# Optimization experiments

Measured on AMD Instinct MI355X. Metric: run time of the kernel, lower is better.

## Reference

```python
import jax, jax.numpy as jnp
import numpy as np

E, W, S, Q, D = 256, 20, 5, 300, 512
ALPHA = 37.0  # hardcoded weight '37' in computeProto


def setup_inputs() -> dict:
    key = jax.random.key(0)
    k1, k2 = jax.random.split(key)
    x_shot = jax.random.normal(k1, (E, W, S, D), dtype=jnp.float32)
    x_query = jax.random.normal(k2, (E, Q, D), dtype=jnp.float32)
    temp = jnp.float32(10.0)
    return {"x_shot": x_shot, "x_query": x_query, "temp": temp}


def compute_proto(x_shot, x_query):
    # x_shot: [E, W, S, D], x_query: [E, Q, D]
    n_shot = x_shot.shape[2]
    shot_sum = x_shot.sum(axis=2)                      # [E, W, D]
    shot_mean = x_shot.mean(axis=2)                    # [E, W, D]
    # pairwise euclidean distance mean-vs-query: [E, W, Q]
    diff = shot_mean[:, :, None, :] - x_query[:, None, :, :]
    dist = jnp.sqrt(jnp.sum(diff * diff, axis=-1))
    weights = jax.nn.softmax(-dist, axis=-1)           # softmax over queries
    pooled = jnp.einsum('ewq,eqd->ewd', weights, x_query)  # [E, W, D]
    proto = (shot_sum + ALPHA * pooled) / (n_shot + ALPHA)
    return proto


def l2norm(x, axis=-1, eps=1e-12):
    n = jnp.sqrt(jnp.sum(x * x, axis=axis, keepdims=True))
    return x / jnp.maximum(n, eps)


def reference(x_shot, x_query, temp):
    proto = compute_proto(x_shot, x_query)             # [E, W, D]
    proto = l2norm(proto)
    q = l2norm(x_query)
    logits = temp * jnp.einsum('eqd,ewd->eqw', q, proto)  # [E, Q, W]
    return logits
```

## Files before the change

kernel.cpp:

```cpp
#include <hip/hip_runtime.h>
#include <math.h>

#define E_ 256
#define W_ 20
#define S_ 5
#define Q_ 300
#define D_ 512
#define ALPHA_ 37.0f
#define QCH 64
#define NCH 5
#define QPAD 304

typedef __attribute__((ext_vector_type(8))) short bf16x8;
typedef __attribute__((ext_vector_type(4))) float f32x4;
typedef __attribute__((ext_vector_type(2))) unsigned int u32x2;
typedef __attribute__((ext_vector_type(4))) unsigned int u32x4;

#define OFF_SS   0
#define OFF_XQ   32768
#define OFF_BUF  98304
#define OFF_Q2   122624
#define OFF_M2   123904
#define OFF_RED  124032
#define LDS_BYTES 124672

__device__ __forceinline__ unsigned short f2bf(float x) {
    unsigned int u = __builtin_bit_cast(unsigned int, x);
    u += 0x7fffu + ((u >> 16) & 1u);
    return (unsigned short)(u >> 16);
}
__device__ __forceinline__ float bf2f(unsigned short h) {
    unsigned int u = ((unsigned int)h) << 16;
    return __builtin_bit_cast(float, u);
}

__device__ __forceinline__ bf16x8 ldfrag(const char* base, int row, int k0) {
    const int phys = (k0 >> 3) ^ (row & 7);
    return *reinterpret_cast<const bf16x8*>(base + row * 1024 + phys * 16);
}

__device__ __forceinline__ void stage_load(const float4* xq4, int c, int qcount,
                                           int tid, float4* r) {
    const int qr = tid >> 3;
    const int i  = tid & 7;
    const int qg = c * QCH + ((qr < qcount) ? qr : 0);
    const float4* row4 = xq4 + (size_t)qg * (D_ / 4);
    #pragma unroll
    for (int j = 0; j < 8; ++j) {
        const int ch = i + 8 * j;
        r[2 * j]     = row4[2 * ch];
        r[2 * j + 1] = row4[2 * ch + 1];
    }
}

template <bool WQ2>
__device__ __forceinline__ void stage_write(const float4* r, char* s_xq, float* s_q2,
                                            int c, int qcount, int tid) {
    const int qr = tid >> 3;
    const int i  = tid & 7;
    const bool valid = qr < qcount;
    float q2 = 0.f;
    #pragma unroll
    for (int j = 0; j < 8; ++j) {
        const int ch = i + 8 * j;
        float4 a = valid ? r[2 * j]     : make_float4(0.f, 0.f, 0.f, 0.f);
        float4 b = valid ? r[2 * j + 1] : make_float4(0.f, 0.f, 0.f, 0.f);
        if (WQ2) {
            q2 += a.x * a.x + a.y * a.y + a.z * a.z + a.w * a.w
                + b.x * b.x + b.y * b.y + b.z * b.z + b.w * b.w;
        }
        u32x4 v;
        v[0] = (unsigned int)f2bf(a.x) | ((unsigned int)f2bf(a.y) << 16);
        v[1] = (unsigned int)f2bf(a.z) | ((unsigned int)f2bf(a.w) << 16);
        v[2] = (unsigned int)f2bf(b.x) | ((unsigned int)f2bf(b.y) << 16);
        v[3] = (unsigned int)f2bf(b.z) | ((unsigned int)f2bf(b.w) << 16);
        *reinterpret_cast<u32x4*>(s_xq + qr * 1024 + ((ch ^ (qr & 7)) << 4)) = v;
    }
    if (WQ2) {
        q2 += __shfl_xor(q2, 1);
        q2 += __shfl_xor(q2, 2);
        q2 += __shfl_xor(q2, 4);
        if (i == 0) s_q2[c * QCH + qr] = valid ? q2 : 0.f;
    }
}

__global__ __launch_bounds__(512) void fused5(const float* __restrict__ xs,
                                              const float* __restrict__ xq,
                                              const float* __restrict__ temp_p,
                                              float* __restrict__ out) {
    extern __shared__ char smem[];
    char*  s_ss  = smem + OFF_SS;
    char*  s_xq  = smem + OFF_XQ;
    float* s_buf = (float*)(smem + OFF_BUF);
    float* s_q2  = (float*)(smem + OFF_Q2);
    float* s_m2  = (float*)(smem + OFF_M2);
    float* s_red = (float*)(smem + OFF_RED);

    const int e    = blockIdx.x;
    const int tid  = threadIdx.x;
    const int lane = tid & 63;
    const int wv   = tid >> 6;
    const int ln15 = lane & 15;
    const int hi   = lane >> 4;

    const float*  xse = xs + (size_t)e * (W_ * S_ * D_);
    const float*  xqe = xq + (size_t)e * (Q_ * D_);
    const float4* xq4 = (const float4*)xqe;
    const float   temp = *temp_p;

    float4 buf[16];

    stage_load(xq4, 0, QCH, tid, buf);

    for (int idx = tid; idx < 12 * 64; idx += 512) {
        const int row = 20 + (idx >> 6), ch = idx & 63;
        u32x4 z = {0u, 0u, 0u, 0u};
        *reinterpret_cast<u32x4*>(s_ss + row * 1024 + ch * 16) = z;
    }
    #pragma unroll
    for (int it = 0; it < 5; ++it) {
        const int idx = it * 512 + tid;
        const int w   = idx >> 7;
        const int dq  = idx & 127;
        const float4* p0 = reinterpret_cast<const float4*>(xse + (w * S_) * D_ + dq * 4);
        float4 a = p0[0];
        #pragma unroll
        for (int s = 1; s < S_; ++s) {
            const float4 t = p0[s * (D_ / 4)];
            a.x += t.x; a.y += t.y; a.z += t.z; a.w += t.w;
        }
        u32x2 v;
        v[0] = (unsigned int)f2bf(a.x) | ((unsigned int)f2bf(a.y) << 16);
        v[1] = (unsigned int)f2bf(a.z) | ((unsigned int)f2bf(a.w) << 16);
        *reinterpret_cast<u32x2*>(s_ss + w * 1024 + (((dq >> 1) ^ (w & 7)) << 4) +
                                  (dq & 1) * 8) = v;
    }
    __syncthreads();

    for (int w = wv; w < W_; w += 8) {
        bf16x8 v = *reinterpret_cast<const bf16x8*>(s_ss + w * 1024 + ((lane ^ (w & 7)) << 4));
        float p = 0.f;
        #pragma unroll
        for (int j = 0; j < 8; ++j) { float f = bf2f((unsigned short)v[j]); p += f * f; }
        #pragma unroll
        for (int off = 32; off; off >>= 1) p += __shfl_xor(p, off);
        if (lane == 0) s_m2[w] = p * (1.f / (S_ * S_));
    }
    __syncthreads();

    for (int c = 0; c < NCH; ++c) {
        const int qcount = (c == 4) ? (Q_ - 4 * QCH) : QCH;
        stage_write<true>(buf, s_xq, s_q2, c, qcount, tid);
        __syncthreads();
        if (c + 1 < NCH)
            stage_load(xq4, c + 1, (c + 1 == 4) ? (Q_ - 4 * QCH) : QCH, tid, buf);

        const int mtile = wv >> 2, ntile = wv & 3;
        f32x4 acc = {0.f, 0.f, 0.f, 0.f};
        const int arow = mtile * 16 + ln15;
        const int brow = ntile * 16 + ln15;
        #pragma unroll
        for (int k = 0; k < 16; ++k) {
            bf16x8 a = ldfrag(s_ss, arow, k * 32 + hi * 8);
            bf16x8 b = ldfrag(s_xq, brow, k * 32 + hi * 8);
            acc = __builtin_amdgcn_mfma_f32_16x16x32_bf16(a, b, acc, 0, 0, 0);
        }
        const int qloc = ntile * 16 + ln15;
        if (qloc < qcount) {
            const int qg = c * QCH + qloc;
            const float q2v = s_q2[qg];
            #pragma unroll
            for (int r = 0; r < 4; ++r) {
                const int w = mtile * 16 + hi * 4 + r;
                if (w < W_) {
                    float d2 = s_m2[w] + q2v - 0.4f * acc[r];
                    s_buf[w * QPAD + qg] = -sqrtf(fmaxf(d2, 0.f));
                }
            }
        }
        __syncthreads();
    }

    for (int w = wv; w < W_; w += 8) {
        float mx = -1e30f;
        for (int q = lane; q < Q_; q += 64) mx = fmaxf(mx, s_buf[w * QPAD + q]);
        #pragma unroll
        for (int off = 32; off; off >>= 1) mx = fmaxf(mx, __shfl_xor(mx, off));
        float sm = 0.f;
        for (int q = lane; q < Q_; q += 64) {
            float ex = __expf(s_buf[w * QPAD + q] - mx);
            s_buf[w * QPAD + q] = ex;
            sm += ex;
        }
        #pragma unroll
        for (int off = 32; off; off >>= 1) sm += __shfl_xor(sm, off);
        const float inv = 1.f / sm;
        for (int q = lane; q < Q_; q += 64) s_buf[w * QPAD + q] *= inv;
    }
    __syncthreads();

    stage_load(xq4, 0, QCH, tid, buf);

    {
        float pr[W_];
        #pragma unroll
        for (int w = 0; w < W_; ++w) pr[w] = 0.f;
        for (int q0 = 0; q0 < Q_; q0 += 4) {
            const float qv0 = xqe[(q0 + 0) * D_ + tid];
            const float qv1 = xqe[(q0 + 1) * D_ + tid];
            const float qv2 = xqe[(q0 + 2) * D_ + tid];
            const float qv3 = xqe[(q0 + 3) * D_ + tid];
            #pragma unroll
            for (int w = 0; w < W_; ++w) {
                const float4 wt = *reinterpret_cast<const float4*>(&s_buf[w * QPAD + q0]);
                pr[w] += wt.x * qv0 + wt.y * qv1 + wt.z * qv2 + wt.w * qv3;
            }
        }
        const int chb = tid >> 3;
        #pragma unroll
        for (int w = 0; w < W_; ++w) {
            unsigned short h =
                *(unsigned short*)(s_ss + w * 1024 + ((chb ^ (w & 7)) << 4) + (tid & 7) * 2);
            pr[w] = (bf2f(h) + ALPHA_ * pr[w]) * (1.f / (S_ + ALPHA_));
        }
        #pragma unroll
        for (int w = 0; w < W_; ++w) {
            float p = pr[w] * pr[w];
            #pragma unroll
            for (int off = 32; off; off >>= 1) p += __shfl_xor(p, off);
            if (lane == 0) s_red[wv * W_ + w] = p;
        }
        __syncthreads();
        if (tid < W_) {
            float p = 0.f;
            #pragma unroll
            for (int k = 0; k < 8; ++k) p += s_red[k * W_ + tid];
            s_m2[tid] = 1.f / fmaxf(sqrtf(p), 1e-12f);
        }
        __syncthreads();
        #pragma unroll
        for (int w = 0; w < W_; ++w) {
            *(unsigned short*)(s_ss + w * 1024 + ((chb ^ (w & 7)) << 4) + (tid & 7) * 2) =
                f2bf(pr[w] * s_m2[w]);
        }
        __syncthreads();
    }

    for (int c = 0; c < NCH; ++c) {
        const int qcount = (c == 4) ? (Q_ - 4 * QCH) : QCH;
        stage_write<false>(buf, s_xq, s_q2, c, qcount, tid);
        __syncthreads();
        if (c + 1 < NCH)
            stage_load(xq4, c + 1, (c + 1 == 4) ? (Q_ - 4 * QCH) : QCH, tid, buf);

        const int mtile = wv >> 1, ntile = wv & 1;
        f32x4 acc = {0.f, 0.f, 0.f, 0.f};
        const int arow = mtile * 16 + ln15;
        const int brow = ntile * 16 + ln15;
        #pragma unroll
        for (int k = 0; k < 16; ++k) {
            bf16x8 a = ldfrag(s_xq, arow, k * 32 + hi * 8);
            bf16x8 b = ldfrag(s_ss, brow, k * 32 + hi * 8);
            acc = __builtin_amdgcn_mfma_f32_16x16x32_bf16(a, b, acc, 0, 0, 0);
        }
        const int w = ntile * 16 + ln15;
        if (w < W_) {
            #pragma unroll
            for (int r = 0; r < 4; ++r) {
                const int qloc = mtile * 16 + hi * 4 + r;
                if (qloc < qcount) {
                    const int qg = c * QCH + qloc;
                    const float scale = temp / fmaxf(sqrtf(s_q2[qg]), 1e-12f);
                    out[(size_t)e * (Q_ * W_) + qg * W_ + w] = scale * acc[r];
                }
            }
        }
        __syncthreads();
    }
}

extern "C" void kernel_launch(void* const* d_in, const int* in_sizes, int n_in,
                              void* d_out, int out_size, void* d_ws, size_t ws_size,
                              hipStream_t stream) {
    const float* xs = (const float*)d_in[0];
    const float* xq = (const float*)d_in[1];
    const float* tp = (const float*)d_in[2];
    hipFuncSetAttribute(reinterpret_cast<const void*>(fused5),
                        hipFuncAttributeMaxDynamicSharedMemorySize, LDS_BYTES);
    fused5<<<E_, 512, LDS_BYTES, stream>>>(xs, xq, tp, (float*)d_out);
}
```

Measured before the change: 109.0 us.

## Split each episode across two blocks by way halves with smaller query chunks

The grid goes from one block per episode to two, each handling 10 of the 20 ways. Query chunks shrink to 32 rows and LDS drops to about 63KB, so more blocks can be resident per CU (launch bounds now request 4). The block index is remapped so consecutive blocks spread across XCDs. In exchange, x_query is read twice per episode, and only 2 of 8 waves do MFMA work per chunk, with twice as many chunk barriers.

```diff
diff --git a/kernel.cpp b/kernel.cpp
--- a/kernel.cpp
+++ b/kernel.cpp
@@ -7,8 +7,9 @@
 #define Q_ 300
 #define D_ 512
 #define ALPHA_ 37.0f
-#define QCH 64
-#define NCH 5
+#define QCH 32
+#define NCH 10
+#define WPB 10
 #define QPAD 304
 
 typedef __attribute__((ext_vector_type(8))) short bf16x8;
@@ -17,12 +18,13 @@
 typedef __attribute__((ext_vector_type(4))) unsigned int u32x4;
 
 #define OFF_SS   0
-#define OFF_XQ   32768
-#define OFF_BUF  98304
-#define OFF_Q2   122624
-#define OFF_M2   123904
-#define OFF_RED  124032
-#define LDS_BYTES 124672
+#define OFF_XQ   16384
+#define OFF_BUF  49152
+#define OFF_Q2   61312
+#define OFF_M2   62592
+#define OFF_MINV 62656
+#define OFF_RED  62720
+#define LDS_BYTES 63040
 
 __device__ __forceinline__ unsigned short f2bf(float x) {
     unsigned int u = __builtin_bit_cast(unsigned int, x);
@@ -41,13 +43,13 @@
 
 __device__ __forceinline__ void stage_load(const float4* xq4, int c, int qcount,
                                            int tid, float4* r) {
-    const int qr = tid >> 3;
-    const int i  = tid & 7;
+    const int qr = tid >> 4;
+    const int i  = tid & 15;
     const int qg = c * QCH + ((qr < qcount) ? qr : 0);
     const float4* row4 = xq4 + (size_t)qg * (D_ / 4);
     #pragma unroll
-    for (int j = 0; j < 8; ++j) {
-        const int ch = i + 8 * j;
+    for (int j = 0; j < 4; ++j) {
+        const int ch = i + 16 * j;
         r[2 * j]     = row4[2 * ch];
         r[2 * j + 1] = row4[2 * ch + 1];
     }
@@ -56,13 +58,13 @@
 template <bool WQ2>
 __device__ __forceinline__ void stage_write(const float4* r, char* s_xq, float* s_q2,
                                             int c, int qcount, int tid) {
-    const int qr = tid >> 3;
-    const int i  = tid & 7;
+    const int qr = tid >> 4;
+    const int i  = tid & 15;
     const bool valid = qr < qcount;
     float q2 = 0.f;
     #pragma unroll
-    for (int j = 0; j < 8; ++j) {
-        const int ch = i + 8 * j;
+    for (int j = 0; j < 4; ++j) {
+        const int ch = i + 16 * j;
         float4 a = valid ? r[2 * j]     : make_float4(0.f, 0.f, 0.f, 0.f);
         float4 b = valid ? r[2 * j + 1] : make_float4(0.f, 0.f, 0.f, 0.f);
         if (WQ2) {
@@ -80,23 +82,29 @@
         q2 += __shfl_xor(q2, 1);
         q2 += __shfl_xor(q2, 2);
         q2 += __shfl_xor(q2, 4);
+        q2 += __shfl_xor(q2, 8);
         if (i == 0) s_q2[c * QCH + qr] = valid ? q2 : 0.f;
     }
 }
 
-__global__ __launch_bounds__(512) void fused5(const float* __restrict__ xs,
-                                              const float* __restrict__ xq,
-                                              const float* __restrict__ temp_p,
-                                              float* __restrict__ out) {
+__global__ __launch_bounds__(512, 4) void fused6(const float* __restrict__ xs,
+                                                 const float* __restrict__ xq,
+                                                 const float* __restrict__ temp_p,
+                                                 float* __restrict__ out) {
     extern __shared__ char smem[];
-    char*  s_ss  = smem + OFF_SS;
-    char*  s_xq  = smem + OFF_XQ;
-    float* s_buf = (float*)(smem + OFF_BUF);
-    float* s_q2  = (float*)(smem + OFF_Q2);
-    float* s_m2  = (float*)(smem + OFF_M2);
-    float* s_red = (float*)(smem + OFF_RED);
-
-    const int e    = blockIdx.x;
+    char*  s_ss   = smem + OFF_SS;
+    char*  s_xq   = smem + OFF_XQ;
+    float* s_buf  = (float*)(smem + OFF_BUF);
+    float* s_q2   = (float*)(smem + OFF_Q2);
+    float* s_m2   = (float*)(smem + OFF_M2);
+    float* s_minv = (float*)(smem + OFF_MINV);
+    float* s_red  = (float*)(smem + OFF_RED);
+
+    const int bid   = blockIdx.x;
+    const int o     = bid >> 3;
+    const int e     = (bid & 7) * 32 + (o & 31);
+    const int wbase = (o >> 5) * WPB;
+
     const int tid  = threadIdx.x;
     const int lane = tid & 63;
     const int wv   = tid >> 6;
@@ -108,170 +116,180 @@
     const float4* xq4 = (const float4*)xqe;
     const float   temp = *temp_p;
 
-    float4 buf[16];
+    float4 buf[8];
 
     stage_load(xq4, 0, QCH, tid, buf);
 
-    for (int idx = tid; idx < 12 * 64; idx += 512) {
-        const int row = 20 + (idx >> 6), ch = idx & 63;
-        u32x4 z = {0u, 0u, 0u, 0u};
-        *reinterpret_cast<u32x4*>(s_ss + row * 1024 + ch * 16) = z;
+    {
+        const int idx = tid;
+        if (idx < 6 * 64) {
+            const int row = WPB + (idx >> 6), ch = idx & 63;
+            u32x4 z = {0u, 0u, 0u, 0u};
+            *reinterpret_cast<u32x4*>(s_ss + row * 1024 + ch * 16) = z;
+        }
     }
     #pragma unroll
-    for (int it = 0; it < 5; ++it) {
+    for (int it = 0; it < 3; ++it) {
         const int idx = it * 512 + tid;
-        const int w   = idx >> 7;
-        const int dq  = idx & 127;
-        const float4* p0 = reinterpret_cast<const float4*>(xse + (w * S_) * D_ + dq * 4);
-        float4 a = p0[0];
-        #pragma unroll
-        for (int s = 1; s < S_; ++s) {
-            const float4 t = p0[s * (D_ / 4)];
-            a.x += t.x; a.y += t.y; a.z += t.z; a.w += t.w;
-        }
-        u32x2 v;
-        v[0] = (unsigned int)f2bf(a.x) | ((unsigned int)f2bf(a.y) << 16);
-        v[1] = (unsigned int)f2bf(a.z) | ((unsigned int)f2bf(a.w) << 16);
-        *reinterpret_cast<u32x2*>(s_ss + w * 1024 + (((dq >> 1) ^ (w & 7)) << 4) +
-                                  (dq & 1) * 8) = v;
+        if (idx < WPB * 128) {
+            const int lw = idx >> 7;
+            const int dq = idx & 127;
+            const int w  = wbase + lw;
+            const float4* p0 = reinterpret_cast<const float4*>(xse + (w * S_) * D_ + dq * 4);
+            float4 a = p0[0];
+            #pragma unroll
+            for (int s = 1; s < S_; ++s) {
+                const float4 t = p0[s * (D_ / 4)];
+                a.x += t.x; a.y += t.y; a.z += t.z; a.w += t.w;
+            }
+            u32x2 v;
+            v[0] = (unsigned int)f2bf(a.x) | ((unsigned int)f2bf(a.y) << 16);
+            v[1] = (unsigned int)f2bf(a.z) | ((unsigned int)f2bf(a.w) << 16);
+            *reinterpret_cast<u32x2*>(s_ss + lw * 1024 + (((dq >> 1) ^ (lw & 7)) << 4) +
+                                      (dq & 1) * 8) = v;
+        }
     }
     __syncthreads();
 
-    for (int w = wv; w < W_; w += 8) {
-        bf16x8 v = *reinterpret_cast<const bf16x8*>(s_ss + w * 1024 + ((lane ^ (w & 7)) << 4));
+    for (int lw = wv; lw < WPB; lw += 8) {
+        bf16x8 v = *reinterpret_cast<const bf16x8*>(s_ss + lw * 1024 + ((lane ^ (lw & 7)) << 4));
         float p = 0.f;
         #pragma unroll
         for (int j = 0; j < 8; ++j) { float f = bf2f((unsigned short)v[j]); p += f * f; }
         #pragma unroll
         for (int off = 32; off; off >>= 1) p += __shfl_xor(p, off);
-        if (lane == 0) s_m2[w] = p * (1.f / (S_ * S_));
+        if (lane == 0) s_m2[lw] = p * (1.f / (S_ * S_));
     }
     __syncthreads();
 
     for (int c = 0; c < NCH; ++c) {
-        const int qcount = (c == 4) ? (Q_ - 4 * QCH) : QCH;
+        const int qcount = (c == NCH - 1) ? (Q_ - (NCH - 1) * QCH) : QCH;
         stage_write<true>(buf, s_xq, s_q2, c, qcount, tid);
         __syncthreads();
         if (c + 1 < NCH)
-            stage_load(xq4, c + 1, (c + 1 == 4) ? (Q_ - 4 * QCH) : QCH, tid, buf);
-
-        const int mtile = wv >> 2, ntile = wv & 3;
-        f32x4 acc = {0.f, 0.f, 0.f, 0.f};
-        const int arow = mtile * 16 + ln15;
-        const int brow = ntile * 16 + ln15;
-        #pragma unroll
-        for (int k = 0; k < 16; ++k) {
-            bf16x8 a = ldfrag(s_ss, arow, k * 32 + hi * 8);
-            bf16x8 b = ldfrag(s_xq, brow, k * 32 + hi * 8);
-            acc = __builtin_amdgcn_mfma_f32_16x16x32_bf16(a, b, acc, 0, 0, 0);
-        }
-        const int qloc = ntile * 16 + ln15;
-        if (qloc < qcount) {
-            const int qg = c * QCH + qloc;
-            const float q2v = s_q2[qg];
-            #pragma unroll
-            for (int r = 0; r < 4; ++r) {
-                const int w = mtile * 16 + hi * 4 + r;
-                if (w < W_) {
-                    float d2 = s_m2[w] + q2v - 0.4f * acc[r];
-                    s_buf[w * QPAD + qg] = -sqrtf(fmaxf(d2, 0.f));
+            stage_load(xq4, c + 1, (c + 2 == NCH) ? (Q_ - (NCH - 1) * QCH) : QCH, tid, buf);
+
+        if (wv < 2) {
+            const int ntile = wv;
+            f32x4 acc = {0.f, 0.f, 0.f, 0.f};
+            const int arow = ln15;
+            const int brow = ntile * 16 + ln15;
+            #pragma unroll
+            for (int k = 0; k < 16; ++k) {
+                bf16x8 a = ldfrag(s_ss, arow, k * 32 + hi * 8);
+                bf16x8 b = ldfrag(s_xq, brow, k * 32 + hi * 8);
+                acc = __builtin_amdgcn_mfma_f32_16x16x32_bf16(a, b, acc, 0, 0, 0);
+            }
+            const int qloc = ntile * 16 + ln15;
+            if (qloc < qcount) {
+                const int qg = c * QCH + qloc;
+                const float q2v = s_q2[qg];
+                #pragma unroll
+                for (int r = 0; r < 4; ++r) {
+                    const int lw = hi * 4 + r;
+                    if (lw < WPB) {
+                        float d2 = s_m2[lw] + q2v - 0.4f * acc[r];
+                        s_buf[lw * QPAD + qg] = -sqrtf(fmaxf(d2, 0.f));
+                    }
                 }
             }
         }
         __syncthreads();
     }
 
-    for (int w = wv; w < W_; w += 8) {
+    for (int lw = wv; lw < WPB; lw += 8) {
         float mx = -1e30f;
-        for (int q = lane; q < Q_; q += 64) mx = fmaxf(mx, s_buf[w * QPAD + q]);
+        for (int q = lane; q < Q_; q += 64) mx = fmaxf(mx, s_buf[lw * QPAD + q]);
         #pragma unroll
         for (int off = 32; off; off >>= 1) mx = fmaxf(mx, __shfl_xor(mx, off));
         float sm = 0.f;
         for (int q = lane; q < Q_; q += 64) {
-            float ex = __expf(s_buf[w * QPAD + q] - mx);
-            s_buf[w * QPAD + q] = ex;
+            float ex = __expf(s_buf[lw * QPAD + q] - mx);
+            s_buf[lw * QPAD + q] = ex;
             sm += ex;
         }
         #pragma unroll
         for (int off = 32; off; off >>= 1) sm += __shfl_xor(sm, off);
         const float inv = 1.f / sm;
-        for (int q = lane; q < Q_; q += 64) s_buf[w * QPAD + q] *= inv;
+        for (int q = lane; q < Q_; q += 64) s_buf[lw * QPAD + q] *= inv;
     }
     __syncthreads();
 
     stage_load(xq4, 0, QCH, tid, buf);
 
     {
-        float pr[W_];
-        #pragma unroll
-        for (int w = 0; w < W_; ++w) pr[w] = 0.f;
+        float pr[WPB];
+        #pragma unroll
+        for (int lw = 0; lw < WPB; ++lw) pr[lw] = 0.f;
         for (int q0 = 0; q0 < Q_; q0 += 4) {
             const float qv0 = xqe[(q0 + 0) * D_ + tid];
             const float qv1 = xqe[(q0 + 1) * D_ + tid];
             const float qv2 = xqe[(q0 + 2) * D_ + tid];
             const float qv3 = xqe[(q0 + 3) * D_ + tid];
             #pragma unroll
-            for (int w = 0; w < W_; ++w) {
-                const float4 wt = *reinterpret_cast<const float4*>(&s_buf[w * QPAD + q0]);
-                pr[w] += wt.x * qv0 + wt.y * qv1 + wt.z * qv2 + wt.w * qv3;
+            for (int lw = 0; lw < WPB; ++lw) {
+                const float4 wt = *reinterpret_cast<const float4*>(&s_buf[lw * QPAD + q0]);
+                pr[lw] += wt.x * qv0 + wt.y * qv1 + wt.z * qv2 + wt.w * qv3;
             }
         }
         const int chb = tid >> 3;
         #pragma unroll
-        for (int w = 0; w < W_; ++w) {
+        for (int lw = 0; lw < WPB; ++lw) {
             unsigned short h =
-                *(unsigned short*)(s_ss + w * 1024 + ((chb ^ (w & 7)) << 4) + (tid & 7) * 2);
-            pr[w] = (bf2f(h) + ALPHA_ * pr[w]) * (1.f / (S_ + ALPHA_));
-        }
-        #pragma unroll
-        for (int w = 0; w < W_; ++w) {
-            float p = pr[w] * pr[w];
+                *(unsigned short*)(s_ss + lw * 1024 + ((chb ^ (lw & 7)) << 4) + (tid & 7) * 2);
+            pr[lw] = (bf2f(h) + ALPHA_ * pr[lw]) * (1.f / (S_ + ALPHA_));
+        }
+        #pragma unroll
+        for (int lw = 0; lw < WPB; ++lw) {
+            float p = pr[lw] * pr[lw];
             #pragma unroll
             for (int off = 32; off; off >>= 1) p += __shfl_xor(p, off);
-            if (lane == 0) s_red[wv * W_ + w] = p;
-        }
-        __syncthreads();
-        if (tid < W_) {
+            if (lane == 0) s_red[wv * WPB + lw] = p;
+        }
+        __syncthreads();
+        if (tid < WPB) {
             float p = 0.f;
             #pragma unroll
-            for (int k = 0; k < 8; ++k) p += s_red[k * W_ + tid];
-            s_m2[tid] = 1.f / fmaxf(sqrtf(p), 1e-12f);
-        }
-        __syncthreads();
-        #pragma unroll
-        for (int w = 0; w < W_; ++w) {
-            *(unsigned short*)(s_ss + w * 1024 + ((chb ^ (w & 7)) << 4) + (tid & 7) * 2) =
-                f2bf(pr[w] * s_m2[w]);
+            for (int k = 0; k < 8; ++k) p += s_red[k * WPB + tid];
+            s_minv[tid] = 1.f / fmaxf(sqrtf(p), 1e-12f);
+        }
+        __syncthreads();
+        #pragma unroll
+        for (int lw = 0; lw < WPB; ++lw) {
+            *(unsigned short*)(s_ss + lw * 1024 + ((chb ^ (lw & 7)) << 4) + (tid & 7) * 2) =
+                f2bf(pr[lw] * s_minv[lw]);
         }
         __syncthreads();
     }
 
     for (int c = 0; c < NCH; ++c) {
-        const int qcount = (c == 4) ? (Q_ - 4 * QCH) : QCH;
+        const int qcount = (c == NCH - 1) ? (Q_ - (NCH - 1) * QCH) : QCH;
         stage_write<false>(buf, s_xq, s_q2, c, qcount, tid);
         __syncthreads();
         if (c + 1 < NCH)
-            stage_load(xq4, c + 1, (c + 1 == 4) ? (Q_ - 4 * QCH) : QCH, tid, buf);
-
-        const int mtile = wv >> 1, ntile = wv & 1;
-        f32x4 acc = {0.f, 0.f, 0.f, 0.f};
-        const int arow = mtile * 16 + ln15;
-        const int brow = ntile * 16 + ln15;
-        #pragma unroll
-        for (int k = 0; k < 16; ++k) {
-            bf16x8 a = ldfrag(s_xq, arow, k * 32 + hi * 8);
-            bf16x8 b = ldfrag(s_ss, brow, k * 32 + hi * 8);
-            acc = __builtin_amdgcn_mfma_f32_16x16x32_bf16(a, b, acc, 0, 0, 0);
-        }
-        const int w = ntile * 16 + ln15;
-        if (w < W_) {
-            #pragma unroll
-            for (int r = 0; r < 4; ++r) {
-                const int qloc = mtile * 16 + hi * 4 + r;
-                if (qloc < qcount) {
-                    const int qg = c * QCH + qloc;
-                    const float scale = temp / fmaxf(sqrtf(s_q2[qg]), 1e-12f);
-                    out[(size_t)e * (Q_ * W_) + qg * W_ + w] = scale * acc[r];
+            stage_load(xq4, c + 1, (c + 2 == NCH) ? (Q_ - (NCH - 1) * QCH) : QCH, tid, buf);
+
+        if (wv < 2) {
+            const int mtile = wv;
+            f32x4 acc = {0.f, 0.f, 0.f, 0.f};
+            const int arow = mtile * 16 + ln15;
+            const int brow = ln15;
+            #pragma unroll
+            for (int k = 0; k < 16; ++k) {
+                bf16x8 a = ldfrag(s_xq, arow, k * 32 + hi * 8);
+                bf16x8 b = ldfrag(s_ss, brow, k * 32 + hi * 8);
+                acc = __builtin_amdgcn_mfma_f32_16x16x32_bf16(a, b, acc, 0, 0, 0);
+            }
+            const int lw = ln15;
+            if (lw < WPB) {
+                #pragma unroll
+                for (int r = 0; r < 4; ++r) {
+                    const int qloc = mtile * 16 + hi * 4 + r;
+                    if (qloc < qcount) {
+                        const int qg = c * QCH + qloc;
+                        const float scale = temp / fmaxf(sqrtf(s_q2[qg]), 1e-12f);
+                        out[(size_t)e * (Q_ * W_) + qg * W_ + wbase + lw] = scale * acc[r];
+                    }
                 }
             }
         }
@@ -285,7 +303,7 @@
     const float* xs = (const float*)d_in[0];
     const float* xq = (const float*)d_in[1];
     const float* tp = (const float*)d_in[2];
-    hipFuncSetAttribute(reinterpret_cast<const void*>(fused5),
+    hipFuncSetAttribute(reinterpret_cast<const void*>(fused6),
                         hipFuncAttributeMaxDynamicSharedMemorySize, LDS_BYTES);
-    fused5<<<E_, 512, LDS_BYTES, stream>>>(xs, xq, tp, (float*)d_out);
-}
+    fused6<<<2 * E_, 512, LDS_BYTES, stream>>>(xs, xq, tp, (float*)d_out);
+}
```

After: 142.3 us. 30.6% more time.

## Keep query bf16 fragments in registers, drop LDS query staging

Applied to the files above, without the earlier changes.

Each wave loads its query tiles directly from global memory into bf16 MFMA fragments held in registers (3 tiles × 16 k-steps). Those fragments are reused for both the distance GEMM and the final logits GEMM, which removes the chunked LDS staging of queries and its per-chunk barriers. LDS use drops from about 124 KB to about 57 KB of static shared memory, and launch bounds request two blocks per CU. The cost is a very large register footprint (192 VGPRs just for fragments, before the 20-float pr array), which may cause spills or prevent the second block per CU.

```diff
diff --git a/kernel.cpp b/kernel.cpp
--- a/kernel.cpp
+++ b/kernel.cpp
@@ -7,23 +7,14 @@
 #define Q_ 300
 #define D_ 512
 #define ALPHA_ 37.0f
-#define QCH 64
-#define NCH 5
 #define QPAD 304
+#define NT 19
 
 typedef __attribute__((ext_vector_type(8))) short bf16x8;
 typedef __attribute__((ext_vector_type(4))) float f32x4;
 typedef __attribute__((ext_vector_type(2))) unsigned int u32x2;
 typedef __attribute__((ext_vector_type(4))) unsigned int u32x4;
 
-#define OFF_SS   0
-#define OFF_XQ   32768
-#define OFF_BUF  98304
-#define OFF_Q2   122624
-#define OFF_M2   123904
-#define OFF_RED  124032
-#define LDS_BYTES 124672
-
 __device__ __forceinline__ unsigned short f2bf(float x) {
     unsigned int u = __builtin_bit_cast(unsigned int, x);
     u += 0x7fffu + ((u >> 16) & 1u);
@@ -39,62 +30,16 @@
     return *reinterpret_cast<const bf16x8*>(base + row * 1024 + phys * 16);
 }
 
-__device__ __forceinline__ void stage_load(const float4* xq4, int c, int qcount,
-                                           int tid, float4* r) {
-    const int qr = tid >> 3;
-    const int i  = tid & 7;
-    const int qg = c * QCH + ((qr < qcount) ? qr : 0);
-    const float4* row4 = xq4 + (size_t)qg * (D_ / 4);
-    #pragma unroll
-    for (int j = 0; j < 8; ++j) {
-        const int ch = i + 8 * j;
-        r[2 * j]     = row4[2 * ch];
-        r[2 * j + 1] = row4[2 * ch + 1];
-    }
-}
-
-template <bool WQ2>
-__device__ __forceinline__ void stage_write(const float4* r, char* s_xq, float* s_q2,
-                                            int c, int qcount, int tid) {
-    const int qr = tid >> 3;
-    const int i  = tid & 7;
-    const bool valid = qr < qcount;
-    float q2 = 0.f;
-    #pragma unroll
-    for (int j = 0; j < 8; ++j) {
-        const int ch = i + 8 * j;
-        float4 a = valid ? r[2 * j]     : make_float4(0.f, 0.f, 0.f, 0.f);
-        float4 b = valid ? r[2 * j + 1] : make_float4(0.f, 0.f, 0.f, 0.f);
-        if (WQ2) {
-            q2 += a.x * a.x + a.y * a.y + a.z * a.z + a.w * a.w
-                + b.x * b.x + b.y * b.y + b.z * b.z + b.w * b.w;
-        }
-        u32x4 v;
-        v[0] = (unsigned int)f2bf(a.x) | ((unsigned int)f2bf(a.y) << 16);
-        v[1] = (unsigned int)f2bf(a.z) | ((unsigned int)f2bf(a.w) << 16);
-        v[2] = (unsigned int)f2bf(b.x) | ((unsigned int)f2bf(b.y) << 16);
-        v[3] = (unsigned int)f2bf(b.z) | ((unsigned int)f2bf(b.w) << 16);
-        *reinterpret_cast<u32x4*>(s_xq + qr * 1024 + ((ch ^ (qr & 7)) << 4)) = v;
-    }
-    if (WQ2) {
-        q2 += __shfl_xor(q2, 1);
-        q2 += __shfl_xor(q2, 2);
-        q2 += __shfl_xor(q2, 4);
-        if (i == 0) s_q2[c * QCH + qr] = valid ? q2 : 0.f;
-    }
-}
-
-__global__ __launch_bounds__(512) void fused5(const float* __restrict__ xs,
-                                              const float* __restrict__ xq,
-                                              const float* __restrict__ temp_p,
-                                              float* __restrict__ out) {
-    extern __shared__ char smem[];
-    char*  s_ss  = smem + OFF_SS;
-    char*  s_xq  = smem + OFF_XQ;
-    float* s_buf = (float*)(smem + OFF_BUF);
-    float* s_q2  = (float*)(smem + OFF_Q2);
-    float* s_m2  = (float*)(smem + OFF_M2);
-    float* s_red = (float*)(smem + OFF_RED);
+__global__ __launch_bounds__(512, 2) void fused7(const float* __restrict__ xs,
+                                                 const float* __restrict__ xq,
+                                                 const float* __restrict__ temp_p,
+                                                 float* __restrict__ out) {
+    __shared__ __align__(16) char  s_ss[32 * 1024];
+    __shared__ __align__(16) float s_buf[W_ * QPAD];
+    __shared__ float s_q2[QPAD];
+    __shared__ float s_m2[32];
+    __shared__ float s_minv[32];
+    __shared__ float s_red[8 * W_];
 
     const int e    = blockIdx.x;
     const int tid  = threadIdx.x;
@@ -103,14 +48,9 @@
     const int ln15 = lane & 15;
     const int hi   = lane >> 4;
 
-    const float*  xse = xs + (size_t)e * (W_ * S_ * D_);
-    const float*  xqe = xq + (size_t)e * (Q_ * D_);
-    const float4* xq4 = (const float4*)xqe;
-    const float   temp = *temp_p;
-
-    float4 buf[16];
-
-    stage_load(xq4, 0, QCH, tid, buf);
+    const float* xse = xs + (size_t)e * (W_ * S_ * D_);
+    const float* xqe = xq + (size_t)e * (Q_ * D_);
+    const float  temp = *temp_p;
 
     for (int idx = tid; idx < 12 * 64; idx += 512) {
         const int row = 20 + (idx >> 6), ch = idx & 63;
@@ -137,6 +77,35 @@
     }
     __syncthreads();
 
+    bf16x8 qf[3][16];
+    #pragma unroll
+    for (int tt = 0; tt < 3; ++tt) {
+        const int tile = wv + tt * 8;
+        if (tile < NT) {
+            const int q  = tile * 16 + ln15;
+            const int qc = (q < Q_) ? q : (Q_ - 1);
+            const float* qrow = xqe + (size_t)qc * D_;
+            float q2 = 0.f;
+            #pragma unroll
+            for (int k = 0; k < 16; ++k) {
+                const int d0 = k * 32 + hi * 8;
+                const float4 a = *reinterpret_cast<const float4*>(qrow + d0);
+                const float4 b = *reinterpret_cast<const float4*>(qrow + d0 + 4);
+                q2 += a.x * a.x + a.y * a.y + a.z * a.z + a.w * a.w
+                    + b.x * b.x + b.y * b.y + b.z * b.z + b.w * b.w;
+                bf16x8 v;
+                v[0] = (short)f2bf(a.x); v[1] = (short)f2bf(a.y);
+                v[2] = (short)f2bf(a.z); v[3] = (short)f2bf(a.w);
+                v[4] = (short)f2bf(b.x); v[5] = (short)f2bf(b.y);
+                v[6] = (short)f2bf(b.z); v[7] = (short)f2bf(b.w);
+                qf[tt][k] = v;
+            }
+            q2 += __shfl_xor(q2, 16);
+            q2 += __shfl_xor(q2, 32);
+            if (hi == 0) s_q2[q] = q2;
+        }
+    }
+
     for (int w = wv; w < W_; w += 8) {
         bf16x8 v = *reinterpret_cast<const bf16x8*>(s_ss + w * 1024 + ((lane ^ (w & 7)) << 4));
         float p = 0.f;
@@ -148,38 +117,37 @@
     }
     __syncthreads();
 
-    for (int c = 0; c < NCH; ++c) {
-        const int qcount = (c == 4) ? (Q_ - 4 * QCH) : QCH;
-        stage_write<true>(buf, s_xq, s_q2, c, qcount, tid);
-        __syncthreads();
-        if (c + 1 < NCH)
-            stage_load(xq4, c + 1, (c + 1 == 4) ? (Q_ - 4 * QCH) : QCH, tid, buf);
-
-        const int mtile = wv >> 2, ntile = wv & 3;
-        f32x4 acc = {0.f, 0.f, 0.f, 0.f};
-        const int arow = mtile * 16 + ln15;
-        const int brow = ntile * 16 + ln15;
-        #pragma unroll
-        for (int k = 0; k < 16; ++k) {
-            bf16x8 a = ldfrag(s_ss, arow, k * 32 + hi * 8);
-            bf16x8 b = ldfrag(s_xq, brow, k * 32 + hi * 8);
-            acc = __builtin_amdgcn_mfma_f32_16x16x32_bf16(a, b, acc, 0, 0, 0);
-        }
-        const int qloc = ntile * 16 + ln15;
-        if (qloc < qcount) {
-            const int qg = c * QCH + qloc;
-            const float q2v = s_q2[qg];
-            #pragma unroll
-            for (int r = 0; r < 4; ++r) {
-                const int w = mtile * 16 + hi * 4 + r;
-                if (w < W_) {
-                    float d2 = s_m2[w] + q2v - 0.4f * acc[r];
-                    s_buf[w * QPAD + qg] = -sqrtf(fmaxf(d2, 0.f));
+    #pragma unroll
+    for (int tt = 0; tt < 3; ++tt) {
+        const int tile = wv + tt * 8;
+        if (tile < NT) {
+            f32x4 acc0 = {0.f, 0.f, 0.f, 0.f};
+            f32x4 acc1 = {0.f, 0.f, 0.f, 0.f};
+            #pragma unroll
+            for (int k = 0; k < 16; ++k) {
+                const bf16x8 a0 = ldfrag(s_ss, ln15,      k * 32 + hi * 8);
+                const bf16x8 a1 = ldfrag(s_ss, 16 + ln15, k * 32 + hi * 8);
+                acc0 = __builtin_amdgcn_mfma_f32_16x16x32_bf16(a0, qf[tt][k], acc0, 0, 0, 0);
+                acc1 = __builtin_amdgcn_mfma_f32_16x16x32_bf16(a1, qf[tt][k], acc1, 0, 0, 0);
+            }
+            const int q = tile * 16 + ln15;
+            if (q < Q_) {
+                const float q2v = s_q2[q];
+                #pragma unroll
+                for (int r = 0; r < 4; ++r) {
+                    const int w0 = hi * 4 + r;
+                    float d2 = s_m2[w0] + q2v - 0.4f * acc0[r];
+                    s_buf[w0 * QPAD + q] = -sqrtf(fmaxf(d2, 0.f));
+                    const int w1 = 16 + hi * 4 + r;
+                    if (w1 < W_) {
+                        float e2 = s_m2[w1] + q2v - 0.4f * acc1[r];
+                        s_buf[w1 * QPAD + q] = -sqrtf(fmaxf(e2, 0.f));
+                    }
                 }
             }
         }
-        __syncthreads();
-    }
+    }
+    __syncthreads();
 
     for (int w = wv; w < W_; w += 8) {
         float mx = -1e30f;
@@ -199,8 +167,6 @@
     }
     __syncthreads();
 
-    stage_load(xq4, 0, QCH, tid, buf);
-
     {
         float pr[W_];
         #pragma unroll
@@ -235,47 +201,42 @@
             float p = 0.f;
             #pragma unroll
             for (int k = 0; k < 8; ++k) p += s_red[k * W_ + tid];
-            s_m2[tid] = 1.f / fmaxf(sqrtf(p), 1e-12f);
+            s_minv[tid] = 1.f / fmaxf(sqrtf(p), 1e-12f);
         }
         __syncthreads();
         #pragma unroll
         for (int w = 0; w < W_; ++w) {
             *(unsigned short*)(s_ss + w * 1024 + ((chb ^ (w & 7)) << 4) + (tid & 7) * 2) =
-                f2bf(pr[w] * s_m2[w]);
+                f2bf(pr[w] * s_minv[w]);
         }
         __syncthreads();
     }
 
-    for (int c = 0; c < NCH; ++c) {
-        const int qcount = (c == 4) ? (Q_ - 4 * QCH) : QCH;
-        stage_write<false>(buf, s_xq, s_q2, c, qcount, tid);
-        __syncthreads();
-        if (c + 1 < NCH)
-            stage_load(xq4, c + 1, (c + 1 == 4) ? (Q_ - 4 * QCH) : QCH, tid, buf);
-
-        const int mtile = wv >> 1, ntile = wv & 1;
-        f32x4 acc = {0.f, 0.f, 0.f, 0.f};
-        const int arow = mtile * 16 + ln15;
-        const int brow = ntile * 16 + ln15;
-        #pragma unroll
-        for (int k = 0; k < 16; ++k) {
-            bf16x8 a = ldfrag(s_xq, arow, k * 32 + hi * 8);
-            bf16x8 b = ldfrag(s_ss, brow, k * 32 + hi * 8);
-            acc = __builtin_amdgcn_mfma_f32_16x16x32_bf16(a, b, acc, 0, 0, 0);
-        }
-        const int w = ntile * 16 + ln15;
-        if (w < W_) {
+    const size_t eoff = (size_t)e * (Q_ * W_);
+    #pragma unroll
+    for (int tt = 0; tt < 3; ++tt) {
+        const int tile = wv + tt * 8;
+        if (tile < NT) {
+            f32x4 acc0 = {0.f, 0.f, 0.f, 0.f};
+            f32x4 acc1 = {0.f, 0.f, 0.f, 0.f};
+            #pragma unroll
+            for (int k = 0; k < 16; ++k) {
+                const bf16x8 b0 = ldfrag(s_ss, ln15,      k * 32 + hi * 8);
+                const bf16x8 b1 = ldfrag(s_ss, 16 + ln15, k * 32 + hi * 8);
+                acc0 = __builtin_amdgcn_mfma_f32_16x16x32_bf16(qf[tt][k], b0, acc0, 0, 0, 0);
+                acc1 = __builtin_amdgcn_mfma_f32_16x16x32_bf16(qf[tt][k], b1, acc1, 0, 0, 0);
+            }
             #pragma unroll
             for (int r = 0; r < 4; ++r) {
-                const int qloc = mtile * 16 + hi * 4 + r;
-                if (qloc < qcount) {
-                    const int qg = c * QCH + qloc;
-                    const float scale = temp / fmaxf(sqrtf(s_q2[qg]), 1e-12f);
-                    out[(size_t)e * (Q_ * W_) + qg * W_ + w] = scale * acc[r];
+                const int q = tile * 16 + hi * 4 + r;
+                if (q < Q_) {
+                    const float scale = temp / fmaxf(sqrtf(s_q2[q]), 1e-12f);
+                    out[eoff + q * W_ + ln15] = scale * acc0[r];
+                    const int w1 = 16 + ln15;
+                    if (w1 < W_) out[eoff + q * W_ + w1] = scale * acc1[r];
                 }
             }
         }
-        __syncthreads();
     }
 }
 
@@ -285,7 +246,5 @@
     const float* xs = (const float*)d_in[0];
     const float* xq = (const float*)d_in[1];
     const float* tp = (const float*)d_in[2];
-    hipFuncSetAttribute(reinterpret_cast<const void*>(fused5),
-                        hipFuncAttributeMaxDynamicSharedMemorySize, LDS_BYTES);
-    fused5<<<E_, 512, LDS_BYTES, stream>>>(xs, xq, tp, (float*)d_out);
-}
+    fused7<<<E_, 512, 0, stream>>>(xs, xq, tp, (float*)d_out);
+}
```

New measurement: 207.9 us. +90.8%, slower.

## Halve query chunk and shrink LDS to fit two blocks per CU

Applied to the files above, without the earlier changes.

Cuts the staged query chunk from 64 to 32 rows and repacks the LDS layout from about 124 KB to about 80 KB. The padded zero rows of the prototype tile are dropped and tile rows overlap instead. The MFMA work per chunk is remapped to four waves using overlapping 4-row W tiles, and launch bounds now request more waves per SIMD so register use drops. The aim is to let two 512-thread blocks share a CU and hide the global-load and barrier latency. In exchange, each block runs twice as many chunk iterations and barriers, and half the waves idle during each MFMA phase.

```diff
diff --git a/kernel.cpp b/kernel.cpp
--- a/kernel.cpp
+++ b/kernel.cpp
@@ -7,8 +7,8 @@
 #define Q_ 300
 #define D_ 512
 #define ALPHA_ 37.0f
-#define QCH 64
-#define NCH 5
+#define QCH 32
+#define NCH 10
 #define QPAD 304
 
 typedef __attribute__((ext_vector_type(8))) short bf16x8;
@@ -17,12 +17,13 @@
 typedef __attribute__((ext_vector_type(4))) unsigned int u32x4;
 
 #define OFF_SS   0
-#define OFF_XQ   32768
-#define OFF_BUF  98304
-#define OFF_Q2   122624
-#define OFF_M2   123904
-#define OFF_RED  124032
-#define LDS_BYTES 124672
+#define OFF_XQ   20480
+#define OFF_BUF  53248
+#define OFF_Q2   77568
+#define OFF_M2   78848
+#define OFF_MINV 78976
+#define OFF_RED  79104
+#define LDS_BYTES 79744
 
 __device__ __forceinline__ unsigned short f2bf(float x) {
     unsigned int u = __builtin_bit_cast(unsigned int, x);
@@ -41,13 +42,13 @@
 
 __device__ __forceinline__ void stage_load(const float4* xq4, int c, int qcount,
                                            int tid, float4* r) {
-    const int qr = tid >> 3;
-    const int i  = tid & 7;
+    const int qr = tid >> 4;
+    const int i  = tid & 15;
     const int qg = c * QCH + ((qr < qcount) ? qr : 0);
     const float4* row4 = xq4 + (size_t)qg * (D_ / 4);
     #pragma unroll
-    for (int j = 0; j < 8; ++j) {
-        const int ch = i + 8 * j;
+    for (int j = 0; j < 4; ++j) {
+        const int ch = i + 16 * j;
         r[2 * j]     = row4[2 * ch];
         r[2 * j + 1] = row4[2 * ch + 1];
     }
@@ -56,13 +57,13 @@
 template <bool WQ2>
 __device__ __forceinline__ void stage_write(const float4* r, char* s_xq, float* s_q2,
                                             int c, int qcount, int tid) {
-    const int qr = tid >> 3;
-    const int i  = tid & 7;
+    const int qr = tid >> 4;
+    const int i  = tid & 15;
     const bool valid = qr < qcount;
     float q2 = 0.f;
     #pragma unroll
-    for (int j = 0; j < 8; ++j) {
-        const int ch = i + 8 * j;
+    for (int j = 0; j < 4; ++j) {
+        const int ch = i + 16 * j;
         float4 a = valid ? r[2 * j]     : make_float4(0.f, 0.f, 0.f, 0.f);
         float4 b = valid ? r[2 * j + 1] : make_float4(0.f, 0.f, 0.f, 0.f);
         if (WQ2) {
@@ -80,21 +81,23 @@
         q2 += __shfl_xor(q2, 1);
         q2 += __shfl_xor(q2, 2);
         q2 += __shfl_xor(q2, 4);
+        q2 += __shfl_xor(q2, 8);
         if (i == 0) s_q2[c * QCH + qr] = valid ? q2 : 0.f;
     }
 }
 
-__global__ __launch_bounds__(512) void fused5(const float* __restrict__ xs,
-                                              const float* __restrict__ xq,
-                                              const float* __restrict__ temp_p,
-                                              float* __restrict__ out) {
+__global__ __launch_bounds__(512, 4) void fused9(const float* __restrict__ xs,
+                                                 const float* __restrict__ xq,
+                                                 const float* __restrict__ temp_p,
+                                                 float* __restrict__ out) {
     extern __shared__ char smem[];
-    char*  s_ss  = smem + OFF_SS;
-    char*  s_xq  = smem + OFF_XQ;
-    float* s_buf = (float*)(smem + OFF_BUF);
-    float* s_q2  = (float*)(smem + OFF_Q2);
-    float* s_m2  = (float*)(smem + OFF_M2);
-    float* s_red = (float*)(smem + OFF_RED);
+    char*  s_ss   = smem + OFF_SS;
+    char*  s_xq   = smem + OFF_XQ;
+    float* s_buf  = (float*)(smem + OFF_BUF);
+    float* s_q2   = (float*)(smem + OFF_Q2);
+    float* s_m2   = (float*)(smem + OFF_M2);
+    float* s_minv = (float*)(smem + OFF_MINV);
+    float* s_red  = (float*)(smem + OFF_RED);
 
     const int e    = blockIdx.x;
     const int tid  = threadIdx.x;
@@ -108,15 +111,10 @@
     const float4* xq4 = (const float4*)xqe;
     const float   temp = *temp_p;
 
-    float4 buf[16];
+    float4 buf[8];
 
     stage_load(xq4, 0, QCH, tid, buf);
 
-    for (int idx = tid; idx < 12 * 64; idx += 512) {
-        const int row = 20 + (idx >> 6), ch = idx & 63;
-        u32x4 z = {0u, 0u, 0u, 0u};
-        *reinterpret_cast<u32x4*>(s_ss + row * 1024 + ch * 16) = z;
-    }
     #pragma unroll
     for (int it = 0; it < 5; ++it) {
         const int idx = it * 512 + tid;
@@ -149,30 +147,30 @@
     __syncthreads();
 
     for (int c = 0; c < NCH; ++c) {
-        const int qcount = (c == 4) ? (Q_ - 4 * QCH) : QCH;
+        const int qcount = (c == NCH - 1) ? (Q_ - (NCH - 1) * QCH) : QCH;
         stage_write<true>(buf, s_xq, s_q2, c, qcount, tid);
         __syncthreads();
         if (c + 1 < NCH)
-            stage_load(xq4, c + 1, (c + 1 == 4) ? (Q_ - 4 * QCH) : QCH, tid, buf);
-
-        const int mtile = wv >> 2, ntile = wv & 3;
-        f32x4 acc = {0.f, 0.f, 0.f, 0.f};
-        const int arow = mtile * 16 + ln15;
-        const int brow = ntile * 16 + ln15;
-        #pragma unroll
-        for (int k = 0; k < 16; ++k) {
-            bf16x8 a = ldfrag(s_ss, arow, k * 32 + hi * 8);
-            bf16x8 b = ldfrag(s_xq, brow, k * 32 + hi * 8);
-            acc = __builtin_amdgcn_mfma_f32_16x16x32_bf16(a, b, acc, 0, 0, 0);
-        }
-        const int qloc = ntile * 16 + ln15;
-        if (qloc < qcount) {
-            const int qg = c * QCH + qloc;
-            const float q2v = s_q2[qg];
-            #pragma unroll
-            for (int r = 0; r < 4; ++r) {
-                const int w = mtile * 16 + hi * 4 + r;
-                if (w < W_) {
+            stage_load(xq4, c + 1, (c + 2 == NCH) ? (Q_ - (NCH - 1) * QCH) : QCH, tid, buf);
+
+        if (wv < 4) {
+            const int wtile = wv >> 1, qtile = wv & 1;
+            f32x4 acc = {0.f, 0.f, 0.f, 0.f};
+            const int arow = wtile * 4 + ln15;
+            const int brow = qtile * 16 + ln15;
+            #pragma unroll
+            for (int k = 0; k < 16; ++k) {
+                bf16x8 a = ldfrag(s_ss, arow, k * 32 + hi * 8);
+                bf16x8 b = ldfrag(s_xq, brow, k * 32 + hi * 8);
+                acc = __builtin_amdgcn_mfma_f32_16x16x32_bf16(a, b, acc, 0, 0, 0);
+            }
+            const int qloc = qtile * 16 + ln15;
+            if (qloc < qcount) {
+                const int qg = c * QCH + qloc;
+                const float q2v = s_q2[qg];
+                #pragma unroll
+                for (int r = 0; r < 4; ++r) {
+                    const int w = wtile * 4 + hi * 4 + r;
                     float d2 = s_m2[w] + q2v - 0.4f * acc[r];
                     s_buf[w * QPAD + qg] = -sqrtf(fmaxf(d2, 0.f));
                 }
@@ -235,43 +233,44 @@
             float p = 0.f;
             #pragma unroll
             for (int k = 0; k < 8; ++k) p += s_red[k * W_ + tid];
-            s_m2[tid] = 1.f / fmaxf(sqrtf(p), 1e-12f);
+            s_minv[tid] = 1.f / fmaxf(sqrtf(p), 1e-12f);
         }
         __syncthreads();
         #pragma unroll
         for (int w = 0; w < W_; ++w) {
             *(unsigned short*)(s_ss + w * 1024 + ((chb ^ (w & 7)) << 4) + (tid & 7) * 2) =
-                f2bf(pr[w] * s_m2[w]);
-        }
-        __syncthreads();
-    }
-
+                f2bf(pr[w] * s_minv[w]);
+        }
+        __syncthreads();
+    }
+
+    const size_t eoff = (size_t)e * (Q_ * W_);
     for (int c = 0; c < NCH; ++c) {
-        const int qcount = (c == 4) ? (Q_ - 4 * QCH) : QCH;
+        const int qcount = (c == NCH - 1) ? (Q_ - (NCH - 1) * QCH) : QCH;
         stage_write<false>(buf, s_xq, s_q2, c, qcount, tid);
         __syncthreads();
         if (c + 1 < NCH)
-            stage_load(xq4, c + 1, (c + 1 == 4) ? (Q_ - 4 * QCH) : QCH, tid, buf);
-
-        const int mtile = wv >> 1, ntile = wv & 1;
-        f32x4 acc = {0.f, 0.f, 0.f, 0.f};
-        const int arow = mtile * 16 + ln15;
-        const int brow = ntile * 16 + ln15;
-        #pragma unroll
-        for (int k = 0; k < 16; ++k) {
-            bf16x8 a = ldfrag(s_xq, arow, k * 32 + hi * 8);
-            bf16x8 b = ldfrag(s_ss, brow, k * 32 + hi * 8);
-            acc = __builtin_amdgcn_mfma_f32_16x16x32_bf16(a, b, acc, 0, 0, 0);
-        }
-        const int w = ntile * 16 + ln15;
-        if (w < W_) {
+            stage_load(xq4, c + 1, (c + 2 == NCH) ? (Q_ - (NCH - 1) * QCH) : QCH, tid, buf);
+
+        if (wv < 4) {
+            const int qtile = wv >> 1, wtile = wv & 1;
+            f32x4 acc = {0.f, 0.f, 0.f, 0.f};
+            const int arow = qtile * 16 + ln15;
+            const int brow = wtile * 4 + ln15;
+            #pragma unroll
+            for (int k = 0; k < 16; ++k) {
+                bf16x8 a = ldfrag(s_xq, arow, k * 32 + hi * 8);
+                bf16x8 b = ldfrag(s_ss, brow, k * 32 + hi * 8);
+                acc = __builtin_amdgcn_mfma_f32_16x16x32_bf16(a, b, acc, 0, 0, 0);
+            }
+            const int w = wtile * 4 + ln15;
             #pragma unroll
             for (int r = 0; r < 4; ++r) {
-                const int qloc = mtile * 16 + hi * 4 + r;
+                const int qloc = qtile * 16 + hi * 4 + r;
                 if (qloc < qcount) {
                     const int qg = c * QCH + qloc;
                     const float scale = temp / fmaxf(sqrtf(s_q2[qg]), 1e-12f);
-                    out[(size_t)e * (Q_ * W_) + qg * W_ + w] = scale * acc[r];
+                    out[eoff + qg * W_ + w] = scale * acc[r];
                 }
             }
         }
@@ -285,7 +284,7 @@
     const float* xs = (const float*)d_in[0];
     const float* xq = (const float*)d_in[1];
     const float* tp = (const float*)d_in[2];
-    hipFuncSetAttribute(reinterpret_cast<const void*>(fused5),
+    hipFuncSetAttribute(reinterpret_cast<const void*>(fused9),
                         hipFuncAttributeMaxDynamicSharedMemorySize, LDS_BYTES);
-    fused5<<<E_, 512, LDS_BYTES, stream>>>(xs, xq, tp, (float*)d_out);
-}
+    fused9<<<E_, 512, LDS_BYTES, stream>>>(xs, xq, tp, (float*)d_out);
+}
```

New measurement: 122.3 us. 12.2% more time.
